# Performance work log

Hardware: AMD Instinct MI355X
Metric: run time of the kernel (lower is better)

The kernel has to match this reference:

```python
import jax, jax.numpy as jnp
import numpy as np

B, S, D, H = 2, 2048, 1024, 16
DH = D // H
DFF = 4 * D
EPS = 1e-5
NEG = -1e9


def _layernorm(x, gamma, beta):
    mu = jnp.mean(x, axis=-1, keepdims=True)
    var = jnp.mean(jnp.square(x - mu), axis=-1, keepdims=True)
    return (x - mu) * jax.lax.rsqrt(var + EPS) * gamma + beta


def setup_inputs() -> dict:
    key = jax.random.key(0)
    ks = jax.random.split(key, 12)
    s = 0.02
    X = jax.random.normal(ks[0], (B, S, D), dtype=jnp.float32)
    # causal mask (True = attend)
    attention_mask = jnp.tril(jnp.ones((S, S), dtype=bool))
    return {
        "X": X,
        "attention_mask": attention_mask,
        "gamma1": jnp.ones((D,), jnp.float32),
        "beta1": jnp.zeros((D,), jnp.float32),
        "Wq": jax.random.normal(ks[1], (H, D, DH), jnp.float32) * s,
        "bq": jnp.zeros((H, DH), jnp.float32),
        "Wk": jax.random.normal(ks[2], (H, D, DH), jnp.float32) * s,
        "bk": jnp.zeros((H, DH), jnp.float32),
        "Wv": jax.random.normal(ks[3], (H, D, DH), jnp.float32) * s,
        "bv": jnp.zeros((H, DH), jnp.float32),
        "W0": jax.random.normal(ks[4], (D, D), jnp.float32) * s,
        "b0": jnp.zeros((D,), jnp.float32),
        "gamma2": jnp.ones((D,), jnp.float32),
        "beta2": jnp.zeros((D,), jnp.float32),
        "W1": jax.random.normal(ks[5], (D, DFF), jnp.float32) * s,
        "b1": jnp.zeros((DFF,), jnp.float32),
        "W2": jax.random.normal(ks[6], (DFF, D), jnp.float32) * s,
        "b2": jnp.zeros((D,), jnp.float32),
    }


def reference(X, attention_mask, gamma1, beta1, Wq, bq, Wk, bk, Wv, bv, W0, b0,
              gamma2, beta2, W1, b1, W2, b2):
    scale = 1.0 / np.sqrt(DH)
    # --- pre-LN MHA ---
    Xn = _layernorm(X, gamma1, beta1)
    # per-head projections, stacked: [B,H,S,DH]
    Q = jnp.einsum('bsd,hdk->bhsk', Xn, Wq) + bq[None, :, None, :]
    K = jnp.einsum('bsd,hdk->bhsk', Xn, Wk) + bk[None, :, None, :]
    V = jnp.einsum('bsd,hdk->bhsk', Xn, Wv) + bv[None, :, None, :]
    scores = jnp.einsum('bhsk,bhtk->bhst', Q, K) * scale
    scores = jnp.where(attention_mask, scores, NEG)
    weights = jax.nn.softmax(scores, axis=-1)
    attn = jnp.einsum('bhst,bhtv->bhsv', weights, V)  # [B,H,S,DH]
    # concat heads (head-major along feature dim, matching torch.cat order)
    attn = attn.transpose(0, 2, 1, 3).reshape(B, S, D)
    mha = attn @ W0 + b0
    X = mha + X  # residual (dropout = identity at eval)
    # --- pre-LN FFN ---
    Xn2 = _layernorm(X, gamma2, beta2)
    h = jax.nn.relu(Xn2 @ W1 + b1)
    ffn = h @ W2 + b2
    return ffn + X
```

## Files before the change

### kernel.cpp

```cpp
#include <hip/hip_runtime.h>
#include <hip/hip_bf16.h>

#define BB 2
#define SS 2048
#define DDIM 1024
#define HH 16
#define DHH 64
#define DFF_ 4096
#define BS 4096
#define NQKV 3072

typedef unsigned short u16;
using short8  = __attribute__((ext_vector_type(8))) short;
using floatx4 = __attribute__((ext_vector_type(4))) float;
using ushort4_t = __attribute__((ext_vector_type(4))) unsigned short;

__device__ __forceinline__ u16 f2b(float f){
  union { unsigned int u; float f; } v; v.f = f;
  unsigned int u = v.u;
  u += 0x7FFFu + ((u >> 16) & 1u);
  return (u16)(u >> 16);
}

__device__ __forceinline__ void gl2lds16(const u16* g, u16* l){
  __builtin_amdgcn_global_load_lds((const __attribute__((address_space(1))) void*)g,
                                   (__attribute__((address_space(3))) void*)l, 16, 0, 0);
}

__device__ __forceinline__ void ln_row(const float* __restrict__ x,
                                       const float* __restrict__ gamma,
                                       const float* __restrict__ beta,
                                       u16* __restrict__ y, int row, float* smem){
  const float4* xr = (const float4*)(x + (size_t)row * DDIM);
  int tid = threadIdx.x;
  float4 v = xr[tid];
  float s  = v.x + v.y + v.z + v.w;
  float ss = v.x*v.x + v.y*v.y + v.z*v.z + v.w*v.w;
  for (int o = 1; o < 64; o <<= 1){ s += __shfl_xor(s, o, 64); ss += __shfl_xor(ss, o, 64); }
  int wid = tid >> 6;
  if ((tid & 63) == 0){ smem[wid] = s; smem[wid + 4] = ss; }
  __syncthreads();
  s  = smem[0] + smem[1] + smem[2] + smem[3];
  ss = smem[4] + smem[5] + smem[6] + smem[7];
  float mu  = s / (float)DDIM;
  float var = ss / (float)DDIM - mu * mu;
  float rs  = rsqrtf(var + 1e-5f);
  const float4* gp = (const float4*)gamma;
  const float4* bp = (const float4*)beta;
  float4 g = gp[tid], b = bp[tid];
  u16* yr = y + (size_t)row * DDIM + tid*4;
  yr[0] = f2b((v.x - mu) * rs * g.x + b.x);
  yr[1] = f2b((v.y - mu) * rs * g.y + b.y);
  yr[2] = f2b((v.z - mu) * rs * g.z + b.z);
  yr[3] = f2b((v.w - mu) * rs * g.w + b.w);
}

__device__ __forceinline__ void tcast(const float* __restrict__ in, u16* __restrict__ out,
                                      int R, int C, int tile, float (*sh)[33]){
  int nr = R >> 5;
  int tr = tile % nr, tc = tile / nr;
  int r0 = tr * 32, c0 = tc * 32;
  int tx = threadIdx.x & 31, ty = threadIdx.x >> 5;
  for (int i = ty; i < 32; i += 8)
    sh[i][tx] = in[(size_t)(r0 + i) * C + c0 + tx];
  __syncthreads();
  for (int i = ty; i < 32; i += 8)
    out[(size_t)(c0 + i) * R + r0 + tx] = f2b(sh[tx][i]);
}

__global__ __launch_bounds__(256) void prep_ln1_k(
    const float* __restrict__ X, const float* __restrict__ g1, const float* __restrict__ be1,
    u16* __restrict__ Xn,
    const float* __restrict__ Wq, const float* __restrict__ Wk, const float* __restrict__ Wv,
    const float* __restrict__ W0, const float* __restrict__ W1,
    const float* __restrict__ bq, const float* __restrict__ bk, const float* __restrict__ bv,
    u16* __restrict__ wqkvT, u16* __restrict__ w0T, u16* __restrict__ w1T,
    float* __restrict__ biasQKV)
{
  __shared__ float sh[32][33];
  __shared__ float smem8[8];
  int id = blockIdx.x;
  if (id < 4096){
    ln_row(X, g1, be1, Xn, id, smem8);
  } else if (id < 7168){
    int lid2 = id - 4096;
    int which = lid2 >> 10, lid = lid2 & 1023;
    const float* src = which == 0 ? Wq : (which == 1 ? Wk : Wv);
    u16* dst = wqkvT + (size_t)which * 1048576;
    int bat = lid >> 6, t = lid & 63;
    tcast(src + (size_t)bat * 65536, dst + (size_t)bat * 65536, 1024, 64, t, sh);
  } else if (id < 8192){
    tcast(W0, w0T, 1024, 1024, id - 7168, sh);
  } else if (id < 12288){
    tcast(W1, w1T, 1024, 4096, id - 8192, sh);
  } else {
    int idx = (id - 12288) * 256 + threadIdx.x;
    if (idx < 3072){
      float v = idx < 1024 ? bq[idx] : (idx < 2048 ? bk[idx - 1024] : bv[idx - 2048]);
      biasQKV[idx] = v;
    }
  }
}

__global__ __launch_bounds__(256) void w2t_ln2_k(
    const float* __restrict__ X1, const float* __restrict__ g2, const float* __restrict__ be2,
    u16* __restrict__ Xn2, const float* __restrict__ W2, u16* __restrict__ w2T)
{
  __shared__ float sh[32][33];
  __shared__ float smem8[8];
  int id = blockIdx.x;
  if (id < 4096){
    ln_row(X1, g2, be2, Xn2, id, smem8);
  } else {
    int tile = id - 4096;
    int tr = tile / 32, tc = tile % 32;
    int r0 = tr * 32, c0 = tc * 32;
    int tx = threadIdx.x & 31, ty = threadIdx.x >> 5;
    for (int i = ty; i < 32; i += 8)
      sh[i][tx] = W2[(size_t)(r0 + i) * 1024 + c0 + tx];
    __syncthreads();
    for (int i = ty; i < 32; i += 8)
      w2T[(size_t)(c0 + i) * 4096 + r0 + tx] = f2b(sh[tx][i]);
  }
}

__global__ __launch_bounds__(256) void vt_k(const u16* __restrict__ QKV, u16* __restrict__ VT){
  __shared__ u16 t[32][33];
  int bh = blockIdx.z; int b = bh >> 4, h = bh & 15;
  int s0 = blockIdx.x * 32, d0 = blockIdx.y * 32;
  int tx = threadIdx.x & 31, ty = threadIdx.x >> 5;
  const u16* src = QKV + (size_t)b * SS * NQKV + 2048 + h * DHH;
  for (int i = ty; i < 32; i += 8)
    t[i][tx] = src[(size_t)(s0 + i) * NQKV + d0 + tx];
  __syncthreads();
  u16* dst = VT + (size_t)bh * DHH * SS;
  for (int i = ty; i < 32; i += 8)
    dst[(size_t)(d0 + i) * SS + s0 + tx] = t[tx][i];
}

template<int TM, int TN, int NP>
__global__ __launch_bounds__(256) void gemm_k(
    const u16* __restrict__ A, const u16* __restrict__ Bt,
    const float* __restrict__ bias, const float* __restrict__ res,
    void* __restrict__ Cv, int M, int N, int K, int relu, int writeBf16)
{
  constexpr int ACH = TM / 16;
  constexpr int BCH = TN / 16;
  constexpr int CH1 = ACH + BCH;
  constexpr int CPW = (NP * CH1) / 4;
  constexpr int MI  = TM / 32;
  constexpr int NI  = TN / 32;

  __shared__ __align__(16) u16 As[NP][TM * 32];
  __shared__ __align__(16) u16 Bs[NP][TN * 32];

  int tid  = threadIdx.x;
  int wave = tid >> 6, lane = tid & 63;
  int quad = lane >> 4, l16 = lane & 15;

  int gx = gridDim.x, gy = gridDim.y;
  int bid = blockIdx.x + gx * blockIdx.y;
  int xcd = bid & 7, idx = bid >> 3;
  int by  = xcd * (gy >> 3) + idx / gx;
  int bx  = idx % gx;

  int m0 = by * TM, n0 = bx * TN;
  int wm = (wave >> 1) * (TM / 2), wn = (wave & 1) * (TN / 2);

  floatx4 acc[MI][NI] = {};

  int srow = lane >> 2;
  int scol = (lane & 3) * 8;
  const u16* gptr[CPW]; u16* lptr[CPW];
#pragma unroll
  for (int k = 0; k < CPW; k++){
    int c = wave * CPW + k;
    int p = c / CH1, cc = c % CH1;
    if (cc < ACH){
      gptr[k] = A  + (size_t)(m0 + cc*16 + srow) * K + p*32 + scol;
      lptr[k] = &As[p][cc * 512];
    } else {
      gptr[k] = Bt + (size_t)(n0 + (cc-ACH)*16 + srow) * K + p*32 + scol;
      lptr[k] = &Bs[p][(cc-ACH) * 512];
    }
  }

  for (int kt = 0; kt < K; kt += NP * 32){
#pragma unroll
    for (int k = 0; k < CPW; k++){ gl2lds16(gptr[k], lptr[k]); gptr[k] += NP * 32; }
    __syncthreads();
#pragma unroll
    for (int p = 0; p < NP; p++){
      short8 af[MI], bf[NI];
#pragma unroll
      for (int i = 0; i < MI; i++)
        af[i] = *(short8*)&As[p][(wm + i*16 + l16)*32 + quad*8];
#pragma unroll
      for (int j = 0; j < NI; j++)
        bf[j] = *(short8*)&Bs[p][(wn + j*16 + l16)*32 + quad*8];
#pragma unroll
      for (int i = 0; i < MI; i++)
#pragma unroll
        for (int j = 0; j < NI; j++)
          acc[i][j] = __builtin_amdgcn_mfma_f32_16x16x32_bf16(bf[j], af[i], acc[i][j], 0,0,0);
    }
    __syncthreads();
  }

  u16*   Cb = (u16*)Cv;
  float* Cf = (float*)Cv;
#pragma unroll
  for (int i = 0; i < MI; i++){
    int row = m0 + wm + i*16 + l16;
#pragma unroll
    for (int j = 0; j < NI; j++){
      int col = n0 + wn + j*16 + quad*4;
      float v0 = acc[i][j][0], v1 = acc[i][j][1], v2 = acc[i][j][2], v3 = acc[i][j][3];
      if (bias){
        const float4 bb = *(const float4*)&bias[col];
        v0 += bb.x; v1 += bb.y; v2 += bb.z; v3 += bb.w;
      }
      if (relu){
        v0 = v0 > 0.f ? v0 : 0.f; v1 = v1 > 0.f ? v1 : 0.f;
        v2 = v2 > 0.f ? v2 : 0.f; v3 = v3 > 0.f ? v3 : 0.f;
      }
      if (res){
        const float4 rr = *(const float4*)&res[(size_t)row * N + col];
        v0 += rr.x; v1 += rr.y; v2 += rr.z; v3 += rr.w;
      }
      if (writeBf16){
        ushort4_t o = { f2b(v0), f2b(v1), f2b(v2), f2b(v3) };
        *(ushort4_t*)&Cb[(size_t)row * N + col] = o;
      } else {
        float4 o; o.x = v0; o.y = v1; o.z = v2; o.w = v3;
        *(float4*)&Cf[(size_t)row * N + col] = o;
      }
    }
  }
}

#define KT   128
#define KsLD 72
#define VTLD 136
#define PsLD 136

__global__ __launch_bounds__(256) void attn_k(
    const u16* __restrict__ QKV, const u16* __restrict__ VT, u16* __restrict__ O)
{
  int bh = blockIdx.x;
  int b = bh >> 4, h = bh & 15;
  int qt = (int)gridDim.y - 1 - blockIdx.y;
  int q0 = qt * 64;
  const u16* Qb_  = QKV + (size_t)b * SS * NQKV + h * DHH;
  const u16* Kb_  = Qb_ + 1024;
  const u16* VTb_ = VT + (size_t)bh * DHH * SS;

  __shared__ __align__(16) u16 Ks [KT * KsLD];
  __shared__ __align__(16) u16 VTs[DHH * VTLD];
  __shared__ __align__(16) u16 Ps [4][16 * PsLD];

  int tid = threadIdx.x;
  int wave = tid >> 6, lane = tid & 63;
  int quad = lane >> 4, l16 = lane & 15;
  int qrow = q0 + wave * 16;

  short8 qf0, qf1;
  {
    const u16* qp = Qb_ + (size_t)(qrow + l16) * NQKV + quad*8;
    qf0 = *(const short8*)qp;
    qf1 = *(const short8*)(qp + 32);
  }

  float l_acc[4] = {0.f, 0.f, 0.f, 0.f};
  floatx4 oacc[4] = {};

  int nk = (qt >> 1) + 1;
  int lim = wave + 4 * (qt & 1);
  const float qs = 0.125f * 1.44269504088896f;

  short8 kreg[4], vreg[4];
#pragma unroll
  for (int it = 0; it < 4; it++){
    int g = tid + it * 256;
    kreg[it] = *(const short8*)(Kb_ + (size_t)(g >> 3) * NQKV + (g & 7) * 8);
    vreg[it] = *(const short8*)(VTb_ + (size_t)(g >> 4) * SS + (g & 15) * 8);
  }

  for (int kt = 0; kt < nk; kt++){
    int k0 = kt * KT;
    __syncthreads();
#pragma unroll
    for (int it = 0; it < 4; it++){
      int g = tid + it * 256;
      *(short8*)&Ks [(g >> 3) * KsLD + (g & 7) * 8]  = kreg[it];
      *(short8*)&VTs[(g >> 4) * VTLD + (g & 15) * 8] = vreg[it];
    }
    __syncthreads();

    if (kt + 1 < nk){
      int kn = k0 + KT;
#pragma unroll
      for (int it = 0; it < 4; it++){
        int g = tid + it * 256;
        kreg[it] = *(const short8*)(Kb_ + (size_t)(kn + (g >> 3)) * NQKV + (g & 7) * 8);
        vreg[it] = *(const short8*)(VTb_ + (size_t)(g >> 4) * SS + kn + (g & 15) * 8);
      }
    }

    bool last = (kt == nk - 1);
    int stmax = last ? lim : 7;
    floatx4 sacc[8] = {};
    __builtin_amdgcn_s_setprio(1);
#pragma unroll
    for (int st = 0; st < 8; st++){
      if (st <= stmax){
        short8 kb0 = *(short8*)&Ks[(st*16 + l16) * KsLD + quad*8];
        short8 kb1 = *(short8*)&Ks[(st*16 + l16) * KsLD + 32 + quad*8];
        sacc[st] = __builtin_amdgcn_mfma_f32_16x16x32_bf16(qf0, kb0, sacc[st], 0,0,0);
        sacc[st] = __builtin_amdgcn_mfma_f32_16x16x32_bf16(qf1, kb1, sacc[st], 0,0,0);
      }
    }
    __builtin_amdgcn_s_setprio(0);

#pragma unroll
    for (int st = 0; st < 8; st++){
      if (st <= stmax){
        if (last){
          int col = k0 + st*16 + l16;
#pragma unroll
          for (int r = 0; r < 4; r++){
            float e = exp2f(sacc[st][r] * qs);
            e = (col <= qrow + quad*4 + r) ? e : 0.f;
            l_acc[r] += e;
            Ps[wave][(quad*4 + r) * PsLD + st*16 + l16] = f2b(e);
          }
        } else {
#pragma unroll
          for (int r = 0; r < 4; r++){
            float e = exp2f(sacc[st][r] * qs);
            l_acc[r] += e;
            Ps[wave][(quad*4 + r) * PsLD + st*16 + l16] = f2b(e);
          }
        }
      } else {
#pragma unroll
        for (int r = 0; r < 4; r++)
          Ps[wave][(quad*4 + r) * PsLD + st*16 + l16] = 0;
      }
    }
    asm volatile("s_waitcnt lgkmcnt(0)" ::: "memory");

    int cmax = last ? (lim >> 1) : 3;
    short8 pa[4];
#pragma unroll
    for (int c = 0; c < 4; c++)
      pa[c] = *(short8*)&Ps[wave][l16 * PsLD + c*32 + quad*8];
    __builtin_amdgcn_s_setprio(1);
#pragma unroll
    for (int ost = 0; ost < 4; ost++){
#pragma unroll
      for (int c = 0; c < 4; c++){
        if (c <= cmax){
          short8 vb = *(short8*)&VTs[(ost*16 + l16) * VTLD + c*32 + quad*8];
          oacc[ost] = __builtin_amdgcn_mfma_f32_16x16x32_bf16(pa[c], vb, oacc[ost], 0,0,0);
        }
      }
    }
    __builtin_amdgcn_s_setprio(0);
  }

#pragma unroll
  for (int r = 0; r < 4; r++){
    for (int o = 1; o < 16; o <<= 1) l_acc[r] += __shfl_xor(l_acc[r], o, 64);
  }
  float inv[4];
#pragma unroll
  for (int r = 0; r < 4; r++) inv[r] = 1.0f / l_acc[r];

#pragma unroll
  for (int ost = 0; ost < 4; ost++)
#pragma unroll
    for (int r = 0; r < 4; r++){
      int s  = qrow + quad*4 + r;
      int dh = ost*16 + l16;
      O[((size_t)b * SS + s) * DDIM + h * DHH + dh] = f2b(oacc[ost][r] * inv[r]);
    }
}

extern "C" void kernel_launch(void* const* d_in, const int* in_sizes, int n_in,
                              void* d_out, int out_size, void* d_ws, size_t ws_size,
                              hipStream_t stream) {
  const float* X   = (const float*)d_in[0];
  const float* g1  = (const float*)d_in[2];
  const float* be1 = (const float*)d_in[3];
  const float* Wq  = (const float*)d_in[4];
  const float* bq  = (const float*)d_in[5];
  const float* Wk  = (const float*)d_in[6];
  const float* bk  = (const float*)d_in[7];
  const float* Wv  = (const float*)d_in[8];
  const float* bv  = (const float*)d_in[9];
  const float* W0  = (const float*)d_in[10];
  const float* b0  = (const float*)d_in[11];
  const float* g2  = (const float*)d_in[12];
  const float* be2 = (const float*)d_in[13];
  const float* W1  = (const float*)d_in[14];
  const float* b1  = (const float*)d_in[15];
  const float* W2  = (const float*)d_in[16];
  const float* b2  = (const float*)d_in[17];
  float* out = (float*)d_out;

  u16* ws16 = (u16*)d_ws;
  u16* wqkvT = ws16;
  u16* w0T   = ws16 + 3145728;
  u16* w2T   = ws16;
  u16* w1T   = ws16 + 4194304;
  u16* QKVb  = ws16 + 8388608;
  u16* VTb   = ws16 + 8388608 + 12582912;
  u16* hb    = ws16 + 8388608;
  u16* Xn    = ws16 + 25165824;
  u16* attnB = Xn;
  float* biasQKV = (float*)(ws16 + 29360128);

  prep_ln1_k<<<dim3(12300), 256, 0, stream>>>(X, g1, be1, Xn,
      Wq, Wk, Wv, W0, W1, bq, bk, bv, wqkvT, w0T, w1T, biasQKV);

  gemm_k<256,128,2><<<dim3(24, 16), 256, 0, stream>>>(Xn, wqkvT, biasQKV, nullptr, QKVb,
      BS, NQKV, 1024, 0, 1);

  vt_k<<<dim3(64, 2, 32), 256, 0, stream>>>(QKVb, VTb);

  attn_k<<<dim3(32, 32), 256, 0, stream>>>(QKVb, VTb, attnB);

  gemm_k<64,128,4><<<dim3(8, 64), 256, 0, stream>>>(attnB, w0T, b0, X, out,
      BS, DDIM, 1024, 0, 0);

  w2t_ln2_k<<<dim3(8192), 256, 0, stream>>>(out, g2, be2, Xn, W2, w2T);

  gemm_k<256,128,2><<<dim3(32, 16), 256, 0, stream>>>(Xn, w1T, b1, nullptr, hb,
      BS, DFF_, 1024, 1, 1);
  gemm_k<64,128,4><<<dim3(8, 64), 256, 0, stream>>>(hb, w2T, b2, out, out,
      BS, DDIM, DFF_, 0, 0);
}
```

Baseline: 437.4 us.

## Double-buffer GEMM LDS tiles to overlap global loads with MFMA

```diff
diff --git a/kernel.cpp b/kernel.cpp
--- a/kernel.cpp
+++ b/kernel.cpp
@@ -138,8 +138,8 @@
     dst[(size_t)(d0 + i) * SS + s0 + tx] = t[tx][i];
 }
 
-template<int TM, int TN, int NP>
-__global__ __launch_bounds__(256) void gemm_k(
+template<int TM, int TN>
+__global__ __launch_bounds__(256) void gemm_db(
     const u16* __restrict__ A, const u16* __restrict__ Bt,
     const float* __restrict__ bias, const float* __restrict__ res,
     void* __restrict__ Cv, int M, int N, int K, int relu, int writeBf16)
@@ -147,12 +147,12 @@
   constexpr int ACH = TM / 16;
   constexpr int BCH = TN / 16;
   constexpr int CH1 = ACH + BCH;
-  constexpr int CPW = (NP * CH1) / 4;
+  constexpr int CPW = (2 * CH1) / 4;
   constexpr int MI  = TM / 32;
   constexpr int NI  = TN / 32;
 
-  __shared__ __align__(16) u16 As[NP][TM * 32];
-  __shared__ __align__(16) u16 Bs[NP][TN * 32];
+  __shared__ __align__(16) u16 As[2][2][TM * 32];
+  __shared__ __align__(16) u16 Bs[2][2][TN * 32];
 
   int tid  = threadIdx.x;
   int wave = tid >> 6, lane = tid & 63;
@@ -171,40 +171,63 @@
 
   int srow = lane >> 2;
   int scol = (lane & 3) * 8;
-  const u16* gptr[CPW]; u16* lptr[CPW];
+  const u16* gptr[CPW]; u16* lp0[CPW]; int lstep[CPW];
 #pragma unroll
   for (int k = 0; k < CPW; k++){
     int c = wave * CPW + k;
     int p = c / CH1, cc = c % CH1;
     if (cc < ACH){
-      gptr[k] = A  + (size_t)(m0 + cc*16 + srow) * K + p*32 + scol;
-      lptr[k] = &As[p][cc * 512];
+      gptr[k]  = A + (size_t)(m0 + cc*16 + srow) * K + p*32 + scol;
+      lp0[k]   = &As[0][p][cc * 512];
+      lstep[k] = 2 * TM * 32;
     } else {
-      gptr[k] = Bt + (size_t)(n0 + (cc-ACH)*16 + srow) * K + p*32 + scol;
-      lptr[k] = &Bs[p][(cc-ACH) * 512];
-    }
-  }
-
-  for (int kt = 0; kt < K; kt += NP * 32){
-#pragma unroll
-    for (int k = 0; k < CPW; k++){ gl2lds16(gptr[k], lptr[k]); gptr[k] += NP * 32; }
-    __syncthreads();
-#pragma unroll
-    for (int p = 0; p < NP; p++){
+      gptr[k]  = Bt + (size_t)(n0 + (cc-ACH)*16 + srow) * K + p*32 + scol;
+      lp0[k]   = &Bs[0][p][(cc-ACH) * 512];
+      lstep[k] = 2 * TN * 32;
+    }
+  }
+
+  int nsteps = K >> 6;
+
+#pragma unroll
+  for (int k = 0; k < CPW; k++){ gl2lds16(gptr[k], lp0[k]); gptr[k] += 64; }
+  asm volatile("s_waitcnt vmcnt(0)" ::: "memory");
+  __builtin_amdgcn_sched_barrier(0);
+  __builtin_amdgcn_s_barrier();
+  __builtin_amdgcn_sched_barrier(0);
+
+  for (int t = 0; t < nsteps; ++t){
+    int cur = t & 1;
+    if (t + 1 < nsteps){
+#pragma unroll
+      for (int k = 0; k < CPW; k++){
+        gl2lds16(gptr[k], lp0[k] + (cur ? 0 : lstep[k]));
+        gptr[k] += 64;
+      }
+    }
+    __builtin_amdgcn_s_setprio(1);
+#pragma unroll
+    for (int p = 0; p < 2; p++){
       short8 af[MI], bf[NI];
 #pragma unroll
       for (int i = 0; i < MI; i++)
-        af[i] = *(short8*)&As[p][(wm + i*16 + l16)*32 + quad*8];
+        af[i] = *(short8*)&As[cur][p][(wm + i*16 + l16)*32 + quad*8];
 #pragma unroll
       for (int j = 0; j < NI; j++)
-        bf[j] = *(short8*)&Bs[p][(wn + j*16 + l16)*32 + quad*8];
+        bf[j] = *(short8*)&Bs[cur][p][(wn + j*16 + l16)*32 + quad*8];
 #pragma unroll
       for (int i = 0; i < MI; i++)
 #pragma unroll
         for (int j = 0; j < NI; j++)
           acc[i][j] = __builtin_amdgcn_mfma_f32_16x16x32_bf16(bf[j], af[i], acc[i][j], 0,0,0);
     }
-    __syncthreads();
+    __builtin_amdgcn_s_setprio(0);
+    if (t + 1 < nsteps){
+      asm volatile("s_waitcnt vmcnt(0)" ::: "memory");
+      __builtin_amdgcn_sched_barrier(0);
+      __builtin_amdgcn_s_barrier();
+      __builtin_amdgcn_sched_barrier(0);
+    }
   }
 
   u16*   Cb = (u16*)Cv;
@@ -424,20 +447,20 @@
   prep_ln1_k<<<dim3(12300), 256, 0, stream>>>(X, g1, be1, Xn,
       Wq, Wk, Wv, W0, W1, bq, bk, bv, wqkvT, w0T, w1T, biasQKV);
 
-  gemm_k<256,128,2><<<dim3(24, 16), 256, 0, stream>>>(Xn, wqkvT, biasQKV, nullptr, QKVb,
+  gemm_db<128,128><<<dim3(24, 32), 256, 0, stream>>>(Xn, wqkvT, biasQKV, nullptr, QKVb,
       BS, NQKV, 1024, 0, 1);
 
   vt_k<<<dim3(64, 2, 32), 256, 0, stream>>>(QKVb, VTb);
 
   attn_k<<<dim3(32, 32), 256, 0, stream>>>(QKVb, VTb, attnB);
 
-  gemm_k<64,128,4><<<dim3(8, 64), 256, 0, stream>>>(attnB, w0T, b0, X, out,
+  gemm_db<64,128><<<dim3(8, 64), 256, 0, stream>>>(attnB, w0T, b0, X, out,
       BS, DDIM, 1024, 0, 0);
 
   w2t_ln2_k<<<dim3(8192), 256, 0, stream>>>(out, g2, be2, Xn, W2, w2T);
 
-  gemm_k<256,128,2><<<dim3(32, 16), 256, 0, stream>>>(Xn, w1T, b1, nullptr, hb,
+  gemm_db<128,128><<<dim3(32, 32), 256, 0, stream>>>(Xn, w1T, b1, nullptr, hb,
       BS, DFF_, 1024, 1, 1);
-  gemm_k<64,128,4><<<dim3(8, 64), 256, 0, stream>>>(hb, w2T, b2, out, out,
+  gemm_db<64,128><<<dim3(8, 64), 256, 0, stream>>>(hb, w2T, b2, out, out,
       BS, DDIM, DFF_, 0, 0);
 }
```

Measured after the change: 370.2 us. 1.18x faster.
